# Optimization experiments

Measured on AMD Instinct MI355X. Metric: run time of the kernel, lower is better.

Reference implementation:

```python
import jax, jax.numpy as jnp
import numpy as np

D_MODEL = 1024
N_HEADS = 16
D_K = D_MODEL // N_HEADS  # 64
ROPE_BASE = 10000.0
MASK_FILL = -1e9


def _rope_cos_sin(seq_len, d_k, dtype):
    # inv_freq over even dims, freqs = outer(t, inv_freq): [S, d_k//2]
    inv_freq = 1.0 / (ROPE_BASE ** (jnp.arange(0, d_k, 2, dtype=jnp.float32) / d_k))
    freqs = jnp.arange(seq_len, dtype=jnp.float32)[:, None] * inv_freq[None, :]
    # broadcast to full d_k (rotate_half convention: same freq for x1 and x2 halves)
    cos = jnp.concatenate([jnp.cos(freqs), jnp.cos(freqs)], axis=-1).astype(dtype)
    sin = jnp.concatenate([jnp.sin(freqs), jnp.sin(freqs)], axis=-1).astype(dtype)
    return cos, sin  # each [S, d_k]


def _apply_rope(x, cos, sin):
    # x: [B, H, S, d_k]; rotate_half: (x1, x2) -> (-x2, x1)
    x1, x2 = jnp.split(x, 2, axis=-1)
    rot = jnp.concatenate([-x2, x1], axis=-1)
    return x * cos[None, None] + rot * sin[None, None]


def setup_inputs() -> dict:
    key = jax.random.key(0)
    kx, kqkv, ko = jax.random.split(key, 3)
    x = jax.random.normal(kx, (1, 4096, D_MODEL), dtype=jnp.float32)
    # nn.Linear weight shape [out, in]; y = x @ W.T
    s = 1.0 / np.sqrt(D_MODEL)
    W_qkv = jax.random.uniform(kqkv, (3 * D_MODEL, D_MODEL), jnp.float32, -s, s)
    W_o = jax.random.uniform(ko, (D_MODEL, D_MODEL), jnp.float32, -s, s)
    return {"x": x, "W_qkv": W_qkv, "W_o": W_o}


def reference(x, W_qkv, W_o):
    B, S, _ = x.shape
    qkv = jnp.einsum("bsd,ed->bse", x, W_qkv)  # [B, S, 3*d_model]
    Q, K, V = jnp.split(qkv, 3, axis=-1)
    # [B, S, H, d_k] -> [B, H, S, d_k]
    reshape = lambda t: t.reshape(B, S, N_HEADS, D_K).transpose(0, 2, 1, 3)
    Q, K, V = reshape(Q), reshape(K), reshape(V)
    cos, sin = _rope_cos_sin(S, D_K, x.dtype)
    Q = _apply_rope(Q, cos, sin)
    K = _apply_rope(K, cos, sin)
    scores = jnp.einsum("bhqd,bhkd->bhqk", Q, K) / jnp.sqrt(jnp.asarray(D_K, x.dtype))
    causal = jnp.tril(jnp.ones((S, S), dtype=bool))
    scores = jnp.where(causal[None, None], scores, jnp.asarray(MASK_FILL, x.dtype))
    attn = jax.nn.softmax(scores, axis=-1)  # dropout inactive at inference
    out = jnp.einsum("bhqk,bhkd->bhqd", attn, V)
    out = out.transpose(0, 2, 1, 3).reshape(B, S, D_MODEL)
    return jnp.einsum("bsd,ed->bse", out, W_o)
```

## Files before the change

kernel.cpp:

```cpp
#include <hip/hip_runtime.h>


typedef __attribute__((ext_vector_type(8)))  short  short8;
typedef __attribute__((ext_vector_type(4)))  float  f32x4;
typedef __attribute__((ext_vector_type(16))) float  f32x16;
typedef __attribute__((ext_vector_type(4)))  float  float4v;
typedef __attribute__((ext_vector_type(4)))  unsigned short ushort4v;
typedef __attribute__((ext_vector_type(4)))  unsigned int   uint4v;

#define S_LEN 4096
#define DMODEL 1024
#define NHEADS 16
#define DKH 64

#define QSCALE 0.18033688011112042f

__device__ __forceinline__ unsigned short f2bf(float f) {
  unsigned u = __builtin_bit_cast(unsigned, f);
  u += 0x7FFFu + ((u >> 16) & 1u);
  return (unsigned short)(u >> 16);
}
__device__ __forceinline__ float bf2f(unsigned short h) {
  return __builtin_bit_cast(float, ((unsigned)h) << 16);
}

#define GLDS16(gsrc, ldst)                                                   \
  __builtin_amdgcn_global_load_lds(                                          \
      (const __attribute__((address_space(1))) void*)(gsrc),                 \
      (__attribute__((address_space(3))) void*)(ldst), 16, 0, 0)

__global__ void cvt_bf16_all(const float* __restrict__ x,    unsigned short* __restrict__ xb,
                             const float* __restrict__ wq,   unsigned short* __restrict__ wqb,
                             const float* __restrict__ wo,   unsigned short* __restrict__ wob) {
  int i = blockIdx.x * blockDim.x + threadIdx.x;
  const float* src; unsigned short* dst; int off;
  if (i < 1048576)               { src = x;  dst = xb;  off = i; }
  else if (i < 1048576 + 786432) { src = wq; dst = wqb; off = i - 1048576; }
  else                           { src = wo; dst = wob; off = i - 1048576 - 786432; }
  float4v v = reinterpret_cast<const float4v*>(src)[off];
  ushort4v o;
  o[0] = f2bf(v[0]); o[1] = f2bf(v[1]); o[2] = f2bf(v[2]); o[3] = f2bf(v[3]);
  reinterpret_cast<ushort4v*>(dst)[off] = o;
}

__global__ void rope_table(float2* __restrict__ tab) {
  int id = blockIdx.x * blockDim.x + threadIdx.x;
  int s = id >> 5, i = id & 31;
  float inv = expf(-(float)(2 * i) * (9.2103403719761836f / 64.0f));
  float ang = (float)s * inv;
  float sn, cs;
  sincosf(ang, &sn, &cs);
  tab[id] = make_float2(cs, sn);
}

__global__ __launch_bounds__(256) void gemm_qkv(const unsigned short* __restrict__ A,
                                                const unsigned short* __restrict__ B,
                                                const float2* __restrict__ tab,
                                                unsigned short* __restrict__ Qr,
                                                unsigned short* __restrict__ Kr,
                                                unsigned short* __restrict__ vtmp) {
  const int K = 1024;
  __shared__ __align__(16) unsigned short As[128 * 32];
  __shared__ __align__(16) unsigned short Bs[128 * 32];

  const int tid = threadIdx.x;
  const int l = tid & 63, w = tid >> 6;
  const int wr = w >> 1, wc = w & 1;
  const int bm = blockIdx.y * 128, bn = blockIdx.x * 128;
  const int lr = l & 15, lk = (l >> 4) * 8;

  f32x4 acc[4][4] = {};

  const unsigned short* Ag0 = A + (size_t)(bm + (tid >> 2)) * K + (tid & 3) * 8;
  const unsigned short* Ag1 = A + (size_t)(bm + 64 + (tid >> 2)) * K + (tid & 3) * 8;
  const unsigned short* Bg0 = B + (size_t)(bn + (tid >> 2)) * K + (tid & 3) * 8;
  const unsigned short* Bg1 = B + (size_t)(bn + 64 + (tid >> 2)) * K + (tid & 3) * 8;
  unsigned short* Ad0 = As + tid * 8;
  unsigned short* Ad1 = As + (tid + 256) * 8;
  unsigned short* Bd0 = Bs + tid * 8;
  unsigned short* Bd1 = Bs + (tid + 256) * 8;

  const unsigned short* Afr = As + (wr * 64 + lr) * 32 + lk;
  const unsigned short* Bfr = Bs + (wc * 64 + lr) * 32 + lk;

  for (int k0 = 0; k0 < K; k0 += 32) {
    GLDS16(Ag0 + k0, Ad0);
    GLDS16(Ag1 + k0, Ad1);
    GLDS16(Bg0 + k0, Bd0);
    GLDS16(Bg1 + k0, Bd1);
    __syncthreads();

    short8 af[4], bfr[4];
#pragma unroll
    for (int mi = 0; mi < 4; mi++) af[mi]  = *(const short8*)(Afr + mi * 16 * 32);
#pragma unroll
    for (int ni = 0; ni < 4; ni++) bfr[ni] = *(const short8*)(Bfr + ni * 16 * 32);

#pragma unroll
    for (int mi = 0; mi < 4; mi++)
#pragma unroll
      for (int ni = 0; ni < 4; ni++)
        acc[mi][ni] = __builtin_amdgcn_mfma_f32_16x16x32_bf16(af[mi], bfr[ni],
                                                              acc[mi][ni], 0, 0, 0);
    __syncthreads();
  }

  const int row0 = bm + wr * 64 + (l >> 4) * 4;
  const int region = bn >> 10;
  if (region < 2) {
    const int base64 = (bn & 1023) + wc * 64;
    const int h = base64 >> 6;
    unsigned short* dst = region ? Kr : Qr;
    const float scale = region ? 1.0f : QSCALE;
    const size_t hb = (size_t)h * S_LEN * DKH;
#pragma unroll
    for (int mi = 0; mi < 4; mi++)
#pragma unroll
      for (int jj = 0; jj < 4; jj++) {
        const int s = row0 + mi * 16 + jj;
        const float2 cs0 = tab[s * 32 + lr];
        const float2 cs1 = tab[s * 32 + lr + 16];
        const float x1 = acc[mi][0][jj], x2 = acc[mi][2][jj];
        const float y1 = acc[mi][1][jj], y2 = acc[mi][3][jj];
        const float o0 = (x1 * cs0.x - x2 * cs0.y) * scale;
        const float o2 = (x2 * cs0.x + x1 * cs0.y) * scale;
        const float o1 = (y1 * cs1.x - y2 * cs1.y) * scale;
        const float o3 = (y2 * cs1.x + y1 * cs1.y) * scale;
        const size_t a = hb + (size_t)s * DKH + lr;
        dst[a]      = f2bf(o0);
        dst[a + 16] = f2bf(o1);
        dst[a + 32] = f2bf(o2);
        dst[a + 48] = f2bf(o3);
      }
  } else {
    const int col0 = (bn - 2048) + wc * 64 + lr;
#pragma unroll
    for (int mi = 0; mi < 4; mi++)
#pragma unroll
      for (int ni = 0; ni < 4; ni++)
#pragma unroll
        for (int jj = 0; jj < 4; jj++)
          vtmp[(size_t)(row0 + mi * 16 + jj) * 1024 + col0 + ni * 16] =
              f2bf(acc[mi][ni][jj]);
  }
}

__global__ __launch_bounds__(256) void gemm_lds_f32(const unsigned short* __restrict__ A,
                                                    const unsigned short* __restrict__ B,
                                                    float* __restrict__ Cp,
                                                    int M, int N, int K) {
  __shared__ __align__(16) unsigned short As[128 * 32];
  __shared__ __align__(16) unsigned short Bs[128 * 32];

  const int tid = threadIdx.x;
  const int l = tid & 63, w = tid >> 6;
  const int wr = w >> 1, wc = w & 1;
  const int bm = blockIdx.y * 128, bn = blockIdx.x * 128;
  const int lr = l & 15, lk = (l >> 4) * 8;

  f32x4 acc[4][4] = {};

  const unsigned short* Ag0 = A + (size_t)(bm + (tid >> 2)) * K + (tid & 3) * 8;
  const unsigned short* Ag1 = A + (size_t)(bm + 64 + (tid >> 2)) * K + (tid & 3) * 8;
  const unsigned short* Bg0 = B + (size_t)(bn + (tid >> 2)) * K + (tid & 3) * 8;
  const unsigned short* Bg1 = B + (size_t)(bn + 64 + (tid >> 2)) * K + (tid & 3) * 8;
  unsigned short* Ad0 = As + tid * 8;
  unsigned short* Ad1 = As + (tid + 256) * 8;
  unsigned short* Bd0 = Bs + tid * 8;
  unsigned short* Bd1 = Bs + (tid + 256) * 8;

  const unsigned short* Afr = As + (wr * 64 + lr) * 32 + lk;
  const unsigned short* Bfr = Bs + (wc * 64 + lr) * 32 + lk;

  for (int k0 = 0; k0 < K; k0 += 32) {
    GLDS16(Ag0 + k0, Ad0);
    GLDS16(Ag1 + k0, Ad1);
    GLDS16(Bg0 + k0, Bd0);
    GLDS16(Bg1 + k0, Bd1);
    __syncthreads();

    short8 af[4], bfr[4];
#pragma unroll
    for (int mi = 0; mi < 4; mi++) af[mi]  = *(const short8*)(Afr + mi * 16 * 32);
#pragma unroll
    for (int ni = 0; ni < 4; ni++) bfr[ni] = *(const short8*)(Bfr + ni * 16 * 32);

#pragma unroll
    for (int mi = 0; mi < 4; mi++)
#pragma unroll
      for (int ni = 0; ni < 4; ni++)
        acc[mi][ni] = __builtin_amdgcn_mfma_f32_16x16x32_bf16(af[mi], bfr[ni],
                                                              acc[mi][ni], 0, 0, 0);
    __syncthreads();
  }

  const int row0 = bm + wr * 64 + (l >> 4) * 4;
  const int col0 = bn + wc * 64 + lr;
#pragma unroll
  for (int mi = 0; mi < 4; mi++)
#pragma unroll
    for (int ni = 0; ni < 4; ni++)
#pragma unroll
      for (int j = 0; j < 4; j++)
        Cp[(size_t)(row0 + mi * 16 + j) * N + (col0 + ni * 16)] = acc[mi][ni][j];
}

__global__ __launch_bounds__(256) void v_transpose(const unsigned short* __restrict__ vtmp,
                                                   unsigned short* __restrict__ Vt) {
  __shared__ unsigned lds[64 * 65];
  const int t  = threadIdx.x;
  const int b  = blockIdx.x;
  const int h  = b >> 6;
  const int s0 = (b & 63) * 64;

  const int sl = t >> 2;
  const int cq = (t & 3) * 16;
  {
    const unsigned short* src = vtmp + (size_t)(s0 + sl) * 1024 + h * 64 + cq;
    short8 v0 = *(const short8*)(src);
    short8 v1 = *(const short8*)(src + 8);
#pragma unroll
    for (int jj = 0; jj < 8; jj++) {
      lds[sl * 65 + cq + jj]     = (unsigned short)v0[jj];
      lds[sl * 65 + cq + 8 + jj] = (unsigned short)v1[jj];
    }
  }
  __syncthreads();

  const int dl = t >> 2;
  const int sq = (t & 3) * 16;
  short8 o0, o1;
#pragma unroll
  for (int k = 0; k < 8; k++) {
    o0[k] = (short)(unsigned short)lds[(sq + k) * 65 + dl];
    o1[k] = (short)(unsigned short)lds[(sq + 8 + k) * 65 + dl];
  }
  unsigned short* dst = Vt + (size_t)(h * 64 + dl) * S_LEN + s0 + sq;
  *(short8*)(dst)     = o0;
  *(short8*)(dst + 8) = o1;
}

__global__ __launch_bounds__(256) void flash_attn_kernel(const unsigned short* __restrict__ Qr,
                                                         const unsigned short* __restrict__ Kr,
                                                         const unsigned short* __restrict__ Vt,
                                                         unsigned short* __restrict__ O) {
  __shared__ __align__(16) char smem[32768];

  const int tid = threadIdx.x;
  const int l  = tid & 63;
  const int w  = tid >> 6;
  const int r  = l & 31;
  const int hi = l >> 5;

  const int bx    = blockIdx.x;
  const int xcd   = bx & 7;
  const int j     = bx >> 3;
  const int h     = xcd * 2 + (j & 1);
  const int qtile = 127 - (j >> 1);
  const int q0    = qtile * 32;

  const unsigned short* Qh = Qr + (size_t)h * S_LEN * DKH;
  const unsigned short* Kh = Kr + (size_t)h * S_LEN * DKH;
  const unsigned short* Vh = Vt + (size_t)h * DKH * S_LEN;

  const int krow  = tid >> 3;
  const int kcE   = (((tid & 7) * 16) ^ ((krow & 7) << 4)) >> 1;
  const size_t kbase = (size_t)krow * DKH + kcE;
  const int vrow  = tid >> 4;
  const int vcE   = (((tid & 15) * 16) ^ ((vrow & 7) << 4)) >> 1;
  const size_t vbase = (size_t)vrow * S_LEN + vcE;

  const int sw      = (r & 7) << 4;
  const int kfbyte  = (w * 32 + r) * 128;
  const int vfbyte0 = r * 256;
  const int vfbyte1 = (r + 32) * 256;
  const int vcol    = w * 64 + hi * 16;

  short8 qf[4];
  {
    const unsigned short* qb = Qh + (size_t)(q0 + r) * 64 + hi * 8;
#pragma unroll
    for (int dc = 0; dc < 4; dc++) qf[dc] = *(const short8*)(qb + dc * 16);
  }

  f32x16 acc0 = {}, acc1 = {};
  float m = -1e30f, lsum = 0.0f;

  const int nwin = (qtile >> 2) + 1;
  for (int it = 0; it < nwin; it++) {
    {
      const unsigned short* Kg = Kh + (size_t)it * 128 * DKH;
      const unsigned short* Vg = Vh + it * 128;
#pragma unroll
      for (int i = 0; i < 4; i++) {
        GLDS16(Kg + kbase + (size_t)i * 32 * DKH, smem + i * 4096 + tid * 16);
        GLDS16(Vg + vbase + (size_t)i * 16 * S_LEN,
               smem + 16384 + i * 4096 + tid * 16);
      }
    }
    __syncthreads();

    const int c = 4 * it + w;
    if (c <= qtile) {
      short8 kf[4], vf[4];
#pragma unroll
      for (int dc = 0; dc < 4; dc++)
        kf[dc] = *(const short8*)(smem + kfbyte + ((dc * 32 + hi * 16) ^ sw));
#pragma unroll
      for (int kc = 0; kc < 2; kc++) {
        vf[kc]     = *(const short8*)(smem + 16384 + vfbyte0 + ((vcol + kc * 32) ^ sw));
        vf[2 + kc] = *(const short8*)(smem + 16384 + vfbyte1 + ((vcol + kc * 32) ^ sw));
      }

      f32x16 st = {};
      __builtin_amdgcn_s_setprio(1);
      st = __builtin_amdgcn_mfma_f32_32x32x16_bf16(kf[0], qf[0], st, 0, 0, 0);
      st = __builtin_amdgcn_mfma_f32_32x32x16_bf16(kf[1], qf[1], st, 0, 0, 0);
      st = __builtin_amdgcn_mfma_f32_32x32x16_bf16(kf[2], qf[2], st, 0, 0, 0);
      st = __builtin_amdgcn_mfma_f32_32x32x16_bf16(kf[3], qf[3], st, 0, 0, 0);
      __builtin_amdgcn_s_setprio(0);

      if (c == qtile) {
#pragma unroll
        for (int reg = 0; reg < 16; reg++) {
          const int koff = (reg & 3) + 8 * (reg >> 2) + 4 * hi;
          if (koff > r) st[reg] = -1e30f;
        }
      }

      float t0 = fmaxf(fmaxf(st[0],  st[1]),  st[2]);
      float t1 = fmaxf(fmaxf(st[3],  st[4]),  st[5]);
      float t2 = fmaxf(fmaxf(st[6],  st[7]),  st[8]);
      float t3 = fmaxf(fmaxf(st[9],  st[10]), st[11]);
      float t4 = fmaxf(fmaxf(st[12], st[13]), st[14]);
      float pm = fmaxf(fmaxf(fmaxf(t0, t1), fmaxf(t2, t3)), fmaxf(t4, st[15]));
      pm = fmaxf(pm, __shfl_xor(pm, 32));

      if (!__all(pm <= m + 8.0f)) {
        float mn  = fmaxf(m, pm);
        float scl = exp2f(m - mn);
        m = mn;
        lsum *= scl;
#pragma unroll
        for (int reg = 0; reg < 16; reg++) { acc0[reg] *= scl; acc1[reg] *= scl; }
      }

      float p[16];
#pragma unroll
      for (int reg = 0; reg < 16; reg++) p[reg] = exp2f(st[reg] - m);

      float s2[8];
#pragma unroll
      for (int i = 0; i < 8; i++) s2[i] = p[2 * i] + p[2 * i + 1];
#pragma unroll
      for (int i = 0; i < 4; i++) s2[i] = s2[i] + s2[i + 4];
      float rs = (s2[0] + s2[2]) + (s2[1] + s2[3]);
      rs += __shfl_xor(rs, 32);
      lsum += rs;

      unsigned wd[8];
#pragma unroll
      for (int i = 0; i < 8; i++) {
        asm("v_cvt_pk_bf16_f32 %0, %1, %2" : "=v"(wd[i]) : "v"(p[2 * i]), "v"(p[2 * i + 1]));
      }
      unsigned pw[8];
#pragma unroll
      for (int i = 0; i < 8; i++) pw[i] = __shfl_xor(wd[i], 32);

      uint4v u0, u1;
      u0[0] = hi ? pw[2] : wd[0];
      u0[1] = hi ? pw[3] : wd[1];
      u0[2] = hi ? wd[2] : pw[0];
      u0[3] = hi ? wd[3] : pw[1];
      u1[0] = hi ? pw[6] : wd[4];
      u1[1] = hi ? pw[7] : wd[5];
      u1[2] = hi ? wd[6] : pw[4];
      u1[3] = hi ? wd[7] : pw[5];
      short8 pa0 = __builtin_bit_cast(short8, u0);
      short8 pa1 = __builtin_bit_cast(short8, u1);

      __builtin_amdgcn_s_setprio(1);
      acc0 = __builtin_amdgcn_mfma_f32_32x32x16_bf16(vf[0], pa0, acc0, 0, 0, 0);
      acc0 = __builtin_amdgcn_mfma_f32_32x32x16_bf16(vf[1], pa1, acc0, 0, 0, 0);
      acc1 = __builtin_amdgcn_mfma_f32_32x32x16_bf16(vf[2], pa0, acc1, 0, 0, 0);
      acc1 = __builtin_amdgcn_mfma_f32_32x32x16_bf16(vf[3], pa1, acc1, 0, 0, 0);
      __builtin_amdgcn_s_setprio(0);
    }
    __syncthreads();
  }

  unsigned (*oaccp)[32][33] = (unsigned (*)[32][33])smem;
  float* mlm = (float*)(smem + 16896);
  float* mll = (float*)(smem + 17408);

  if (hi == 0) { mlm[w * 32 + r] = m; mll[w * 32 + r] = lsum; }
#pragma unroll
  for (int i = 0; i < 8; i++) {
    const int widx = 4 * (i >> 1) + 2 * hi + (i & 1);
    unsigned ua, ub;
    asm("v_cvt_pk_bf16_f32 %0, %1, %2" : "=v"(ua) : "v"(acc0[2 * i]), "v"(acc0[2 * i + 1]));
    asm("v_cvt_pk_bf16_f32 %0, %1, %2" : "=v"(ub) : "v"(acc1[2 * i]), "v"(acc1[2 * i + 1]));
    oaccp[w][r][widx]      = ua;
    oaccp[w][r][16 + widx] = ub;
  }
  __syncthreads();

  const int q  = tid >> 3;
  const int c0 = (tid & 7) * 4;
  const float m0 = mlm[q], m1 = mlm[32 + q], m2 = mlm[64 + q], m3 = mlm[96 + q];
  const float mmax = fmaxf(fmaxf(m0, m1), fmaxf(m2, m3));
  const float sc[4] = {exp2f(m0 - mmax), exp2f(m1 - mmax),
                       exp2f(m2 - mmax), exp2f(m3 - mmax)};
  const float ltot = sc[0] * mll[q] + sc[1] * mll[32 + q] +
                     sc[2] * mll[64 + q] + sc[3] * mll[96 + q];
  const float rinv = 1.0f / ltot;

  float vs[8] = {};
#pragma unroll
  for (int wv = 0; wv < 4; wv++) {
#pragma unroll
    for (int i = 0; i < 4; i++) {
      unsigned u = oaccp[wv][q][c0 + i];
      vs[2 * i]     += sc[wv] * __builtin_bit_cast(float, u << 16);
      vs[2 * i + 1] += sc[wv] * __builtin_bit_cast(float, u & 0xFFFF0000u);
    }
  }
  short8 ov;
#pragma unroll
  for (int i = 0; i < 8; i++) ov[i] = (short)f2bf(vs[i] * rinv);
  *(short8*)(O + (size_t)(q0 + q) * DMODEL + h * 64 + c0 * 2) = ov;
}

extern "C" void kernel_launch(void* const* d_in, const int* in_sizes, int n_in,
                              void* d_out, int out_size, void* d_ws, size_t ws_size,
                              hipStream_t stream) {
  (void)in_sizes; (void)n_in; (void)out_size; (void)ws_size;
  const float* x    = (const float*)d_in[0];
  const float* Wqkv = (const float*)d_in[1];
  const float* Wo   = (const float*)d_in[2];
  float* out = (float*)d_out;

  char* ws = (char*)d_ws;
  const size_t MB = 1u << 20;
  unsigned short* x_bf    = (unsigned short*)(ws + 0 * MB);
  unsigned short* wqkv_bf = (unsigned short*)(ws + 8 * MB);
  unsigned short* wo_bf   = (unsigned short*)(ws + 14 * MB);
  unsigned short* vtmp    = (unsigned short*)(ws + 16 * MB);
  float2*         tab     = (float2*)(ws + 24 * MB);
  unsigned short* Qr      = (unsigned short*)(ws + 40 * MB);
  unsigned short* Kr      = (unsigned short*)(ws + 48 * MB);
  unsigned short* Vt      = (unsigned short*)(ws + 56 * MB);
  unsigned short* Obf     = (unsigned short*)(ws + 64 * MB);

  cvt_bf16_all<<<8192, 256, 0, stream>>>(x, x_bf, Wqkv, wqkv_bf, Wo, wo_bf);
  rope_table<<<512, 256, 0, stream>>>(tab);

  gemm_qkv<<<dim3(3072 / 128, 4096 / 128), 256, 0, stream>>>(x_bf, wqkv_bf, tab,
                                                             Qr, Kr, vtmp);
  v_transpose<<<1024, 256, 0, stream>>>(vtmp, Vt);

  flash_attn_kernel<<<2048, 256, 0, stream>>>(Qr, Kr, Vt, Obf);

  gemm_lds_f32<<<dim3(1024 / 128, 4096 / 128), 256, 0, stream>>>(Obf, wo_bf, out,
                                                                 4096, 1024, 1024);
}
```

Before: 185.4 us.

## Double-buffer K/V tiles and split flash-attention block into two query tiles

Each block now covers 64 queries using two wave pairs, and each wave pair splits the keys of a 64-key window. The 64-key K/V windows are double-buffered in LDS, with the next window's global-to-LDS loads issued before the current window is computed, so load latency overlaps with MFMA work. The final combine merges two partial softmax states per query row instead of four. This halves the grid, which reduces parallelism across CUs, and spreads the per-window K/V reuse over two query tiles.

After: 177.6 us. -4.2%, faster.

```diff
diff --git a/kernel.cpp b/kernel.cpp
--- a/kernel.cpp
+++ b/kernel.cpp
@@ -244,41 +244,44 @@
                                                          const unsigned short* __restrict__ Kr,
                                                          const unsigned short* __restrict__ Vt,
                                                          unsigned short* __restrict__ O) {
-  __shared__ __align__(16) char smem[32768];
+  __shared__ __align__(16) char smem[2][16384];
 
   const int tid = threadIdx.x;
   const int l  = tid & 63;
   const int w  = tid >> 6;
   const int r  = l & 31;
   const int hi = l >> 5;
+  const int wsub = w >> 1;
+  const int wpar = w & 1;
 
   const int bx    = blockIdx.x;
   const int xcd   = bx & 7;
   const int j     = bx >> 3;
   const int h     = xcd * 2 + (j & 1);
-  const int qtile = 127 - (j >> 1);
-  const int q0    = qtile * 32;
+  const int jj    = 63 - (j >> 1);
+  const int q0    = jj * 64;
 
   const unsigned short* Qh = Qr + (size_t)h * S_LEN * DKH;
   const unsigned short* Kh = Kr + (size_t)h * S_LEN * DKH;
   const unsigned short* Vh = Vt + (size_t)h * DKH * S_LEN;
 
-  const int krow  = tid >> 3;
-  const int kcE   = (((tid & 7) * 16) ^ ((krow & 7) << 4)) >> 1;
-  const size_t kbase = (size_t)krow * DKH + kcE;
-  const int vrow  = tid >> 4;
-  const int vcE   = (((tid & 15) * 16) ^ ((vrow & 7) << 4)) >> 1;
-  const size_t vbase = (size_t)vrow * S_LEN + vcE;
+  const int qtile_w = 2 * jj + wsub;
+  const int qbase   = q0 + wsub * 32;
+
+  const int srow = tid >> 3;
+  const int scol = (((tid & 7) * 16) ^ ((srow & 7) << 4)) >> 1;
+  const size_t kbase = (size_t)srow * DKH + scol;
+  const size_t vbase = (size_t)srow * S_LEN + scol;
 
   const int sw      = (r & 7) << 4;
-  const int kfbyte  = (w * 32 + r) * 128;
-  const int vfbyte0 = r * 256;
-  const int vfbyte1 = (r + 32) * 256;
-  const int vcol    = w * 64 + hi * 16;
+  const int kfbyte  = (wpar * 32 + r) * 128;
+  const int vfbyte0 = r * 128;
+  const int vfbyte1 = (r + 32) * 128;
+  const int vcol    = wpar * 64 + hi * 16;
 
   short8 qf[4];
   {
-    const unsigned short* qb = Qh + (size_t)(q0 + r) * 64 + hi * 8;
+    const unsigned short* qb = Qh + (size_t)(qbase + r) * 64 + hi * 8;
 #pragma unroll
     for (int dc = 0; dc < 4; dc++) qf[dc] = *(const short8*)(qb + dc * 16);
   }
@@ -286,30 +289,39 @@
   f32x16 acc0 = {}, acc1 = {};
   float m = -1e30f, lsum = 0.0f;
 
-  const int nwin = (qtile >> 2) + 1;
+  const int nwin = jj + 1;
+
+#pragma unroll
+  for (int i = 0; i < 2; i++) {
+    GLDS16(Kh + kbase + (size_t)i * 32 * DKH,   smem[0] + i * 4096 + tid * 16);
+    GLDS16(Vh + vbase + (size_t)i * 32 * S_LEN, smem[0] + 8192 + i * 4096 + tid * 16);
+  }
+  __syncthreads();
+
+  int buf = 0;
   for (int it = 0; it < nwin; it++) {
-    {
-      const unsigned short* Kg = Kh + (size_t)it * 128 * DKH;
-      const unsigned short* Vg = Vh + it * 128;
-#pragma unroll
-      for (int i = 0; i < 4; i++) {
-        GLDS16(Kg + kbase + (size_t)i * 32 * DKH, smem + i * 4096 + tid * 16);
-        GLDS16(Vg + vbase + (size_t)i * 16 * S_LEN,
-               smem + 16384 + i * 4096 + tid * 16);
+    if (it + 1 < nwin) {
+      char* sd = smem[buf ^ 1];
+      const unsigned short* Kg = Kh + (size_t)(it + 1) * 64 * DKH;
+      const unsigned short* Vg = Vh + (size_t)(it + 1) * 64;
+#pragma unroll
+      for (int i = 0; i < 2; i++) {
+        GLDS16(Kg + kbase + (size_t)i * 32 * DKH,   sd + i * 4096 + tid * 16);
+        GLDS16(Vg + vbase + (size_t)i * 32 * S_LEN, sd + 8192 + i * 4096 + tid * 16);
       }
     }
-    __syncthreads();
-
-    const int c = 4 * it + w;
-    if (c <= qtile) {
+
+    const char* sm = smem[buf];
+    const int c = 2 * it + wpar;
+    if (c <= qtile_w) {
       short8 kf[4], vf[4];
 #pragma unroll
       for (int dc = 0; dc < 4; dc++)
-        kf[dc] = *(const short8*)(smem + kfbyte + ((dc * 32 + hi * 16) ^ sw));
+        kf[dc] = *(const short8*)(sm + kfbyte + ((dc * 32 + hi * 16) ^ sw));
 #pragma unroll
       for (int kc = 0; kc < 2; kc++) {
-        vf[kc]     = *(const short8*)(smem + 16384 + vfbyte0 + ((vcol + kc * 32) ^ sw));
-        vf[2 + kc] = *(const short8*)(smem + 16384 + vfbyte1 + ((vcol + kc * 32) ^ sw));
+        vf[kc]     = *(const short8*)(sm + 8192 + vfbyte0 + ((vcol + kc * 32) ^ sw));
+        vf[2 + kc] = *(const short8*)(sm + 8192 + vfbyte1 + ((vcol + kc * 32) ^ sw));
       }
 
       f32x16 st = {};
@@ -320,7 +332,7 @@
       st = __builtin_amdgcn_mfma_f32_32x32x16_bf16(kf[3], qf[3], st, 0, 0, 0);
       __builtin_amdgcn_s_setprio(0);
 
-      if (c == qtile) {
+      if (c == qtile_w) {
 #pragma unroll
         for (int reg = 0; reg < 16; reg++) {
           const int koff = (reg & 3) + 8 * (reg >> 2) + 4 * hi;
@@ -386,12 +398,14 @@
       acc1 = __builtin_amdgcn_mfma_f32_32x32x16_bf16(vf[3], pa1, acc1, 0, 0, 0);
       __builtin_amdgcn_s_setprio(0);
     }
+
     __syncthreads();
+    buf ^= 1;
   }
 
   unsigned (*oaccp)[32][33] = (unsigned (*)[32][33])smem;
-  float* mlm = (float*)(smem + 16896);
-  float* mll = (float*)(smem + 17408);
+  float* mlm = (float*)((char*)smem + 16896);
+  float* mll = (float*)((char*)smem + 17408);
 
   if (hi == 0) { mlm[w * 32 + r] = m; mll[w * 32 + r] = lsum; }
 #pragma unroll
@@ -405,30 +419,37 @@
   }
   __syncthreads();
 
-  const int q  = tid >> 3;
-  const int c0 = (tid & 7) * 4;
-  const float m0 = mlm[q], m1 = mlm[32 + q], m2 = mlm[64 + q], m3 = mlm[96 + q];
-  const float mmax = fmaxf(fmaxf(m0, m1), fmaxf(m2, m3));
-  const float sc[4] = {exp2f(m0 - mmax), exp2f(m1 - mmax),
-                       exp2f(m2 - mmax), exp2f(m3 - mmax)};
-  const float ltot = sc[0] * mll[q] + sc[1] * mll[32 + q] +
-                     sc[2] * mll[64 + q] + sc[3] * mll[96 + q];
+  const int st  = tid >> 7;
+  const int rem = tid & 127;
+  const int q   = rem >> 2;
+  const int c0  = (rem & 3) * 8;
+  const int w0  = 2 * st, w1 = 2 * st + 1;
+
+  const float m0 = mlm[w0 * 32 + q], m1 = mlm[w1 * 32 + q];
+  const float mmax = fmaxf(m0, m1);
+  const float sc0 = exp2f(m0 - mmax), sc1 = exp2f(m1 - mmax);
+  const float ltot = sc0 * mll[w0 * 32 + q] + sc1 * mll[w1 * 32 + q];
   const float rinv = 1.0f / ltot;
 
-  float vs[8] = {};
-#pragma unroll
-  for (int wv = 0; wv < 4; wv++) {
-#pragma unroll
-    for (int i = 0; i < 4; i++) {
-      unsigned u = oaccp[wv][q][c0 + i];
-      vs[2 * i]     += sc[wv] * __builtin_bit_cast(float, u << 16);
-      vs[2 * i + 1] += sc[wv] * __builtin_bit_cast(float, u & 0xFFFF0000u);
-    }
-  }
-  short8 ov;
-#pragma unroll
-  for (int i = 0; i < 8; i++) ov[i] = (short)f2bf(vs[i] * rinv);
-  *(short8*)(O + (size_t)(q0 + q) * DMODEL + h * 64 + c0 * 2) = ov;
+  float vs[16];
+#pragma unroll
+  for (int i = 0; i < 8; i++) {
+    unsigned ua = oaccp[w0][q][c0 + i];
+    unsigned ub = oaccp[w1][q][c0 + i];
+    vs[2 * i]     = sc0 * __builtin_bit_cast(float, ua << 16)
+                  + sc1 * __builtin_bit_cast(float, ub << 16);
+    vs[2 * i + 1] = sc0 * __builtin_bit_cast(float, ua & 0xFFFF0000u)
+                  + sc1 * __builtin_bit_cast(float, ub & 0xFFFF0000u);
+  }
+  short8 ov0, ov1;
+#pragma unroll
+  for (int i = 0; i < 8; i++) {
+    ov0[i] = (short)f2bf(vs[i] * rinv);
+    ov1[i] = (short)f2bf(vs[8 + i] * rinv);
+  }
+  unsigned short* op = O + (size_t)(q0 + st * 32 + q) * DMODEL + h * 64 + c0 * 2;
+  *(short8*)(op)     = ov0;
+  *(short8*)(op + 8) = ov1;
 }
 
 extern "C" void kernel_launch(void* const* d_in, const int* in_sizes, int n_in,
@@ -459,7 +480,7 @@
                                                              Qr, Kr, vtmp);
   v_transpose<<<1024, 256, 0, stream>>>(vtmp, Vt);
 
-  flash_attn_kernel<<<2048, 256, 0, stream>>>(Qr, Kr, Vt, Obf);
+  flash_attn_kernel<<<1024, 256, 0, stream>>>(Qr, Kr, Vt, Obf);
 
   gemm_lds_f32<<<dim3(1024 / 128, 4096 / 128), 256, 0, stream>>>(Obf, wo_bf, out,
                                                                  4096, 1024, 1024);
```

## Fuse rope table into cvt, write V transposed in GEMM, pair causal tiles

Applied to the files above, without the earlier changes.

The RoPE table generation moves into the bf16 conversion kernel, and the QKV GEMM now writes V directly in transposed [head, d, seq] layout with 4-element packed stores. This removes the separate rope_table and v_transpose launches along with the vtmp round trip. The flash attention kernel launches half as many blocks, and each block handles two query tiles (tp and 127-tp) so causal work per block is balanced. The costs are strided 8-byte stores for V and longer-running attention blocks with less parallelism per launch.

Result: slower. 201.3 us (+8.6%).

```diff
diff --git a/kernel.cpp b/kernel.cpp
--- a/kernel.cpp
+++ b/kernel.cpp
@@ -29,28 +29,32 @@
       (const __attribute__((address_space(1))) void*)(gsrc),                 \
       (__attribute__((address_space(3))) void*)(ldst), 16, 0, 0)
 
+#define CVT_TOTAL (1048576 + 786432 + 262144)
 __global__ void cvt_bf16_all(const float* __restrict__ x,    unsigned short* __restrict__ xb,
                              const float* __restrict__ wq,   unsigned short* __restrict__ wqb,
-                             const float* __restrict__ wo,   unsigned short* __restrict__ wob) {
+                             const float* __restrict__ wo,   unsigned short* __restrict__ wob,
+                             float2* __restrict__ tab) {
   int i = blockIdx.x * blockDim.x + threadIdx.x;
-  const float* src; unsigned short* dst; int off;
-  if (i < 1048576)               { src = x;  dst = xb;  off = i; }
-  else if (i < 1048576 + 786432) { src = wq; dst = wqb; off = i - 1048576; }
-  else                           { src = wo; dst = wob; off = i - 1048576 - 786432; }
-  float4v v = reinterpret_cast<const float4v*>(src)[off];
-  ushort4v o;
-  o[0] = f2bf(v[0]); o[1] = f2bf(v[1]); o[2] = f2bf(v[2]); o[3] = f2bf(v[3]);
-  reinterpret_cast<ushort4v*>(dst)[off] = o;
-}
-
-__global__ void rope_table(float2* __restrict__ tab) {
-  int id = blockIdx.x * blockDim.x + threadIdx.x;
-  int s = id >> 5, i = id & 31;
-  float inv = expf(-(float)(2 * i) * (9.2103403719761836f / 64.0f));
-  float ang = (float)s * inv;
-  float sn, cs;
-  sincosf(ang, &sn, &cs);
-  tab[id] = make_float2(cs, sn);
+  if (i < CVT_TOTAL) {
+    const float* src; unsigned short* dst; int off;
+    if (i < 1048576)               { src = x;  dst = xb;  off = i; }
+    else if (i < 1048576 + 786432) { src = wq; dst = wqb; off = i - 1048576; }
+    else                           { src = wo; dst = wob; off = i - 1048576 - 786432; }
+    float4v v = reinterpret_cast<const float4v*>(src)[off];
+    ushort4v o;
+    o[0] = f2bf(v[0]); o[1] = f2bf(v[1]); o[2] = f2bf(v[2]); o[3] = f2bf(v[3]);
+    reinterpret_cast<ushort4v*>(dst)[off] = o;
+  } else {
+    int id = i - CVT_TOTAL;
+    if (id < S_LEN * 32) {
+      int s = id >> 5, fi = id & 31;
+      float inv = expf(-(float)(2 * fi) * (9.2103403719761836f / 64.0f));
+      float ang = (float)s * inv;
+      float sn, cs;
+      sincosf(ang, &sn, &cs);
+      tab[id] = make_float2(cs, sn);
+    }
+  }
 }
 
 __global__ __launch_bounds__(256) void gemm_qkv(const unsigned short* __restrict__ A,
@@ -58,7 +62,7 @@
                                                 const float2* __restrict__ tab,
                                                 unsigned short* __restrict__ Qr,
                                                 unsigned short* __restrict__ Kr,
-                                                unsigned short* __restrict__ vtmp) {
+                                                unsigned short* __restrict__ Vt) {
   const int K = 1024;
   __shared__ __align__(16) unsigned short As[128 * 32];
   __shared__ __align__(16) unsigned short Bs[128 * 32];
@@ -133,15 +137,23 @@
         dst[a + 48] = f2bf(o3);
       }
   } else {
-    const int col0 = (bn - 2048) + wc * 64 + lr;
-#pragma unroll
-    for (int mi = 0; mi < 4; mi++)
-#pragma unroll
-      for (int ni = 0; ni < 4; ni++)
-#pragma unroll
-        for (int jj = 0; jj < 4; jj++)
-          vtmp[(size_t)(row0 + mi * 16 + jj) * 1024 + col0 + ni * 16] =
-              f2bf(acc[mi][ni][jj]);
+    const int colh = (bn - 2048) + wc * 64;
+    const int h = colh >> 6;
+    unsigned short* base = Vt + (size_t)h * DKH * S_LEN;
+#pragma unroll
+    for (int mi = 0; mi < 4; mi++) {
+      const int s = row0 + mi * 16;
+#pragma unroll
+      for (int ni = 0; ni < 4; ni++) {
+        const int d = ni * 16 + lr;
+        ushort4v pk;
+        pk[0] = f2bf(acc[mi][ni][0]);
+        pk[1] = f2bf(acc[mi][ni][1]);
+        pk[2] = f2bf(acc[mi][ni][2]);
+        pk[3] = f2bf(acc[mi][ni][3]);
+        *(ushort4v*)(base + (size_t)d * S_LEN + s) = pk;
+      }
+    }
   }
 }
 
@@ -205,41 +217,6 @@
         Cp[(size_t)(row0 + mi * 16 + j) * N + (col0 + ni * 16)] = acc[mi][ni][j];
 }
 
-__global__ __launch_bounds__(256) void v_transpose(const unsigned short* __restrict__ vtmp,
-                                                   unsigned short* __restrict__ Vt) {
-  __shared__ unsigned lds[64 * 65];
-  const int t  = threadIdx.x;
-  const int b  = blockIdx.x;
-  const int h  = b >> 6;
-  const int s0 = (b & 63) * 64;
-
-  const int sl = t >> 2;
-  const int cq = (t & 3) * 16;
-  {
-    const unsigned short* src = vtmp + (size_t)(s0 + sl) * 1024 + h * 64 + cq;
-    short8 v0 = *(const short8*)(src);
-    short8 v1 = *(const short8*)(src + 8);
-#pragma unroll
-    for (int jj = 0; jj < 8; jj++) {
-      lds[sl * 65 + cq + jj]     = (unsigned short)v0[jj];
-      lds[sl * 65 + cq + 8 + jj] = (unsigned short)v1[jj];
-    }
-  }
-  __syncthreads();
-
-  const int dl = t >> 2;
-  const int sq = (t & 3) * 16;
-  short8 o0, o1;
-#pragma unroll
-  for (int k = 0; k < 8; k++) {
-    o0[k] = (short)(unsigned short)lds[(sq + k) * 65 + dl];
-    o1[k] = (short)(unsigned short)lds[(sq + 8 + k) * 65 + dl];
-  }
-  unsigned short* dst = Vt + (size_t)(h * 64 + dl) * S_LEN + s0 + sq;
-  *(short8*)(dst)     = o0;
-  *(short8*)(dst + 8) = o1;
-}
-
 __global__ __launch_bounds__(256) void flash_attn_kernel(const unsigned short* __restrict__ Qr,
                                                          const unsigned short* __restrict__ Kr,
                                                          const unsigned short* __restrict__ Vt,
@@ -252,12 +229,11 @@
   const int r  = l & 31;
   const int hi = l >> 5;
 
-  const int bx    = blockIdx.x;
-  const int xcd   = bx & 7;
-  const int j     = bx >> 3;
-  const int h     = xcd * 2 + (j & 1);
-  const int qtile = 127 - (j >> 1);
-  const int q0    = qtile * 32;
+  const int bx  = blockIdx.x;
+  const int xcd = bx & 7;
+  const int j   = bx >> 3;
+  const int h   = xcd * 2 + (j & 1);
+  const int tp  = j >> 1;
 
   const unsigned short* Qh = Qr + (size_t)h * S_LEN * DKH;
   const unsigned short* Kh = Kr + (size_t)h * S_LEN * DKH;
@@ -276,159 +252,166 @@
   const int vfbyte1 = (r + 32) * 256;
   const int vcol    = w * 64 + hi * 16;
 
-  short8 qf[4];
-  {
-    const unsigned short* qb = Qh + (size_t)(q0 + r) * 64 + hi * 8;
-#pragma unroll
-    for (int dc = 0; dc < 4; dc++) qf[dc] = *(const short8*)(qb + dc * 16);
-  }
-
-  f32x16 acc0 = {}, acc1 = {};
-  float m = -1e30f, lsum = 0.0f;
-
-  const int nwin = (qtile >> 2) + 1;
-  for (int it = 0; it < nwin; it++) {
+  for (int phase = 0; phase < 2; phase++) {
+    const int sub  = phase ? (127 - tp) : tp;
+    const int q0   = sub * 32;
+    const int nwin = (sub >> 2) + 1;
+
+    short8 qf[4];
     {
-      const unsigned short* Kg = Kh + (size_t)it * 128 * DKH;
-      const unsigned short* Vg = Vh + it * 128;
-#pragma unroll
-      for (int i = 0; i < 4; i++) {
-        GLDS16(Kg + kbase + (size_t)i * 32 * DKH, smem + i * 4096 + tid * 16);
-        GLDS16(Vg + vbase + (size_t)i * 16 * S_LEN,
-               smem + 16384 + i * 4096 + tid * 16);
-      }
-    }
-    __syncthreads();
-
-    const int c = 4 * it + w;
-    if (c <= qtile) {
-      short8 kf[4], vf[4];
-#pragma unroll
-      for (int dc = 0; dc < 4; dc++)
-        kf[dc] = *(const short8*)(smem + kfbyte + ((dc * 32 + hi * 16) ^ sw));
-#pragma unroll
-      for (int kc = 0; kc < 2; kc++) {
-        vf[kc]     = *(const short8*)(smem + 16384 + vfbyte0 + ((vcol + kc * 32) ^ sw));
-        vf[2 + kc] = *(const short8*)(smem + 16384 + vfbyte1 + ((vcol + kc * 32) ^ sw));
-      }
-
-      f32x16 st = {};
-      __builtin_amdgcn_s_setprio(1);
-      st = __builtin_amdgcn_mfma_f32_32x32x16_bf16(kf[0], qf[0], st, 0, 0, 0);
-      st = __builtin_amdgcn_mfma_f32_32x32x16_bf16(kf[1], qf[1], st, 0, 0, 0);
-      st = __builtin_amdgcn_mfma_f32_32x32x16_bf16(kf[2], qf[2], st, 0, 0, 0);
-      st = __builtin_amdgcn_mfma_f32_32x32x16_bf16(kf[3], qf[3], st, 0, 0, 0);
-      __builtin_amdgcn_s_setprio(0);
-
-      if (c == qtile) {
-#pragma unroll
-        for (int reg = 0; reg < 16; reg++) {
-          const int koff = (reg & 3) + 8 * (reg >> 2) + 4 * hi;
-          if (koff > r) st[reg] = -1e30f;
+      const unsigned short* qb = Qh + (size_t)(q0 + r) * 64 + hi * 8;
+#pragma unroll
+      for (int dc = 0; dc < 4; dc++) qf[dc] = *(const short8*)(qb + dc * 16);
+    }
+
+    f32x16 acc0 = {}, acc1 = {};
+    float m = -1e30f, lsum = 0.0f;
+
+    for (int it = 0; it < nwin; it++) {
+      {
+        const unsigned short* Kg = Kh + (size_t)it * 128 * DKH;
+        const unsigned short* Vg = Vh + it * 128;
+#pragma unroll
+        for (int i = 0; i < 4; i++) {
+          GLDS16(Kg + kbase + (size_t)i * 32 * DKH, smem + i * 4096 + tid * 16);
+          GLDS16(Vg + vbase + (size_t)i * 16 * S_LEN,
+                 smem + 16384 + i * 4096 + tid * 16);
         }
       }
-
-      float t0 = fmaxf(fmaxf(st[0],  st[1]),  st[2]);
-      float t1 = fmaxf(fmaxf(st[3],  st[4]),  st[5]);
-      float t2 = fmaxf(fmaxf(st[6],  st[7]),  st[8]);
-      float t3 = fmaxf(fmaxf(st[9],  st[10]), st[11]);
-      float t4 = fmaxf(fmaxf(st[12], st[13]), st[14]);
-      float pm = fmaxf(fmaxf(fmaxf(t0, t1), fmaxf(t2, t3)), fmaxf(t4, st[15]));
-      pm = fmaxf(pm, __shfl_xor(pm, 32));
-
-      if (!__all(pm <= m + 8.0f)) {
-        float mn  = fmaxf(m, pm);
-        float scl = exp2f(m - mn);
-        m = mn;
-        lsum *= scl;
-#pragma unroll
-        for (int reg = 0; reg < 16; reg++) { acc0[reg] *= scl; acc1[reg] *= scl; }
+      __syncthreads();
+
+      const int c = 4 * it + w;
+      if (c <= sub) {
+        short8 kf[4], vf[4];
+#pragma unroll
+        for (int dc = 0; dc < 4; dc++)
+          kf[dc] = *(const short8*)(smem + kfbyte + ((dc * 32 + hi * 16) ^ sw));
+#pragma unroll
+        for (int kc = 0; kc < 2; kc++) {
+          vf[kc]     = *(const short8*)(smem + 16384 + vfbyte0 + ((vcol + kc * 32) ^ sw));
+          vf[2 + kc] = *(const short8*)(smem + 16384 + vfbyte1 + ((vcol + kc * 32) ^ sw));
+        }
+
+        f32x16 st = {};
+        __builtin_amdgcn_s_setprio(1);
+        st = __builtin_amdgcn_mfma_f32_32x32x16_bf16(kf[0], qf[0], st, 0, 0, 0);
+        st = __builtin_amdgcn_mfma_f32_32x32x16_bf16(kf[1], qf[1], st, 0, 0, 0);
+        st = __builtin_amdgcn_mfma_f32_32x32x16_bf16(kf[2], qf[2], st, 0, 0, 0);
+        st = __builtin_amdgcn_mfma_f32_32x32x16_bf16(kf[3], qf[3], st, 0, 0, 0);
+        __builtin_amdgcn_s_setprio(0);
+
+        if (c == sub) {
+#pragma unroll
+          for (int reg = 0; reg < 16; reg++) {
+            const int koff = (reg & 3) + 8 * (reg >> 2) + 4 * hi;
+            if (koff > r) st[reg] = -1e30f;
+          }
+        }
+
+        float t0 = fmaxf(fmaxf(st[0],  st[1]),  st[2]);
+        float t1 = fmaxf(fmaxf(st[3],  st[4]),  st[5]);
+        float t2 = fmaxf(fmaxf(st[6],  st[7]),  st[8]);
+        float t3 = fmaxf(fmaxf(st[9],  st[10]), st[11]);
+        float t4 = fmaxf(fmaxf(st[12], st[13]), st[14]);
+        float pm = fmaxf(fmaxf(fmaxf(t0, t1), fmaxf(t2, t3)), fmaxf(t4, st[15]));
+        pm = fmaxf(pm, __shfl_xor(pm, 32));
+
+        if (!__all(pm <= m + 8.0f)) {
+          float mn  = fmaxf(m, pm);
+          float scl = exp2f(m - mn);
+          m = mn;
+          lsum *= scl;
+#pragma unroll
+          for (int reg = 0; reg < 16; reg++) { acc0[reg] *= scl; acc1[reg] *= scl; }
+        }
+
+        float p2[16];
+#pragma unroll
+        for (int reg = 0; reg < 16; reg++) p2[reg] = exp2f(st[reg] - m);
+
+        float s2[8];
+#pragma unroll
+        for (int i = 0; i < 8; i++) s2[i] = p2[2 * i] + p2[2 * i + 1];
+#pragma unroll
+        for (int i = 0; i < 4; i++) s2[i] = s2[i] + s2[i + 4];
+        float rs = (s2[0] + s2[2]) + (s2[1] + s2[3]);
+        rs += __shfl_xor(rs, 32);
+        lsum += rs;
+
+        unsigned wd[8];
+#pragma unroll
+        for (int i = 0; i < 8; i++) {
+          asm("v_cvt_pk_bf16_f32 %0, %1, %2" : "=v"(wd[i]) : "v"(p2[2 * i]), "v"(p2[2 * i + 1]));
+        }
+        unsigned pw[8];
+#pragma unroll
+        for (int i = 0; i < 8; i++) pw[i] = __shfl_xor(wd[i], 32);
+
+        uint4v u0, u1;
+        u0[0] = hi ? pw[2] : wd[0];
+        u0[1] = hi ? pw[3] : wd[1];
+        u0[2] = hi ? wd[2] : pw[0];
+        u0[3] = hi ? wd[3] : pw[1];
+        u1[0] = hi ? pw[6] : wd[4];
+        u1[1] = hi ? pw[7] : wd[5];
+        u1[2] = hi ? wd[6] : pw[4];
+        u1[3] = hi ? wd[7] : pw[5];
+        short8 pa0 = __builtin_bit_cast(short8, u0);
+        short8 pa1 = __builtin_bit_cast(short8, u1);
+
+        __builtin_amdgcn_s_setprio(1);
+        acc0 = __builtin_amdgcn_mfma_f32_32x32x16_bf16(vf[0], pa0, acc0, 0, 0, 0);
+        acc0 = __builtin_amdgcn_mfma_f32_32x32x16_bf16(vf[1], pa1, acc0, 0, 0, 0);
+        acc1 = __builtin_amdgcn_mfma_f32_32x32x16_bf16(vf[2], pa0, acc1, 0, 0, 0);
+        acc1 = __builtin_amdgcn_mfma_f32_32x32x16_bf16(vf[3], pa1, acc1, 0, 0, 0);
+        __builtin_amdgcn_s_setprio(0);
       }
-
-      float p[16];
-#pragma unroll
-      for (int reg = 0; reg < 16; reg++) p[reg] = exp2f(st[reg] - m);
-
-      float s2[8];
-#pragma unroll
-      for (int i = 0; i < 8; i++) s2[i] = p[2 * i] + p[2 * i + 1];
-#pragma unroll
-      for (int i = 0; i < 4; i++) s2[i] = s2[i] + s2[i + 4];
-      float rs = (s2[0] + s2[2]) + (s2[1] + s2[3]);
-      rs += __shfl_xor(rs, 32);
-      lsum += rs;
-
-      unsigned wd[8];
-#pragma unroll
-      for (int i = 0; i < 8; i++) {
-        asm("v_cvt_pk_bf16_f32 %0, %1, %2" : "=v"(wd[i]) : "v"(p[2 * i]), "v"(p[2 * i + 1]));
+      __syncthreads();
+    }
+
+    unsigned (*oaccp)[32][33] = (unsigned (*)[32][33])smem;
+    float* mlm = (float*)(smem + 16896);
+    float* mll = (float*)(smem + 17408);
+
+    if (hi == 0) { mlm[w * 32 + r] = m; mll[w * 32 + r] = lsum; }
+#pragma unroll
+    for (int i = 0; i < 8; i++) {
+      const int widx = 4 * (i >> 1) + 2 * hi + (i & 1);
+      unsigned ua, ub;
+      asm("v_cvt_pk_bf16_f32 %0, %1, %2" : "=v"(ua) : "v"(acc0[2 * i]), "v"(acc0[2 * i + 1]));
+      asm("v_cvt_pk_bf16_f32 %0, %1, %2" : "=v"(ub) : "v"(acc1[2 * i]), "v"(acc1[2 * i + 1]));
+      oaccp[w][r][widx]      = ua;
+      oaccp[w][r][16 + widx] = ub;
+    }
+    __syncthreads();
+
+    const int q  = tid >> 3;
+    const int c0 = (tid & 7) * 4;
+    const float m0 = mlm[q], m1 = mlm[32 + q], m2 = mlm[64 + q], m3 = mlm[96 + q];
+    const float mmax = fmaxf(fmaxf(m0, m1), fmaxf(m2, m3));
+    const float sc[4] = {exp2f(m0 - mmax), exp2f(m1 - mmax),
+                         exp2f(m2 - mmax), exp2f(m3 - mmax)};
+    const float ltot = sc[0] * mll[q] + sc[1] * mll[32 + q] +
+                       sc[2] * mll[64 + q] + sc[3] * mll[96 + q];
+    const float rinv = 1.0f / ltot;
+
+    float vs[8] = {};
+#pragma unroll
+    for (int wv = 0; wv < 4; wv++) {
+#pragma unroll
+      for (int i = 0; i < 4; i++) {
+        unsigned u = oaccp[wv][q][c0 + i];
+        vs[2 * i]     += sc[wv] * __builtin_bit_cast(float, u << 16);
+        vs[2 * i + 1] += sc[wv] * __builtin_bit_cast(float, u & 0xFFFF0000u);
       }
-      unsigned pw[8];
-#pragma unroll
-      for (int i = 0; i < 8; i++) pw[i] = __shfl_xor(wd[i], 32);
-
-      uint4v u0, u1;
-      u0[0] = hi ? pw[2] : wd[0];
-      u0[1] = hi ? pw[3] : wd[1];
-      u0[2] = hi ? wd[2] : pw[0];
-      u0[3] = hi ? wd[3] : pw[1];
-      u1[0] = hi ? pw[6] : wd[4];
-      u1[1] = hi ? pw[7] : wd[5];
-      u1[2] = hi ? wd[6] : pw[4];
-      u1[3] = hi ? wd[7] : pw[5];
-      short8 pa0 = __builtin_bit_cast(short8, u0);
-      short8 pa1 = __builtin_bit_cast(short8, u1);
-
-      __builtin_amdgcn_s_setprio(1);
-      acc0 = __builtin_amdgcn_mfma_f32_32x32x16_bf16(vf[0], pa0, acc0, 0, 0, 0);
-      acc0 = __builtin_amdgcn_mfma_f32_32x32x16_bf16(vf[1], pa1, acc0, 0, 0, 0);
-      acc1 = __builtin_amdgcn_mfma_f32_32x32x16_bf16(vf[2], pa0, acc1, 0, 0, 0);
-      acc1 = __builtin_amdgcn_mfma_f32_32x32x16_bf16(vf[3], pa1, acc1, 0, 0, 0);
-      __builtin_amdgcn_s_setprio(0);
-    }
+    }
+    short8 ov;
+#pragma unroll
+    for (int i = 0; i < 8; i++) ov[i] = (short)f2bf(vs[i] * rinv);
+    *(short8*)(O + (size_t)(q0 + q) * DMODEL + h * 64 + c0 * 2) = ov;
+
     __syncthreads();
   }
-
-  unsigned (*oaccp)[32][33] = (unsigned (*)[32][33])smem;
-  float* mlm = (float*)(smem + 16896);
-  float* mll = (float*)(smem + 17408);
-
-  if (hi == 0) { mlm[w * 32 + r] = m; mll[w * 32 + r] = lsum; }
-#pragma unroll
-  for (int i = 0; i < 8; i++) {
-    const int widx = 4 * (i >> 1) + 2 * hi + (i & 1);
-    unsigned ua, ub;
-    asm("v_cvt_pk_bf16_f32 %0, %1, %2" : "=v"(ua) : "v"(acc0[2 * i]), "v"(acc0[2 * i + 1]));
-    asm("v_cvt_pk_bf16_f32 %0, %1, %2" : "=v"(ub) : "v"(acc1[2 * i]), "v"(acc1[2 * i + 1]));
-    oaccp[w][r][widx]      = ua;
-    oaccp[w][r][16 + widx] = ub;
-  }
-  __syncthreads();
-
-  const int q  = tid >> 3;
-  const int c0 = (tid & 7) * 4;
-  const float m0 = mlm[q], m1 = mlm[32 + q], m2 = mlm[64 + q], m3 = mlm[96 + q];
-  const float mmax = fmaxf(fmaxf(m0, m1), fmaxf(m2, m3));
-  const float sc[4] = {exp2f(m0 - mmax), exp2f(m1 - mmax),
-                       exp2f(m2 - mmax), exp2f(m3 - mmax)};
-  const float ltot = sc[0] * mll[q] + sc[1] * mll[32 + q] +
-                     sc[2] * mll[64 + q] + sc[3] * mll[96 + q];
-  const float rinv = 1.0f / ltot;
-
-  float vs[8] = {};
-#pragma unroll
-  for (int wv = 0; wv < 4; wv++) {
-#pragma unroll
-    for (int i = 0; i < 4; i++) {
-      unsigned u = oaccp[wv][q][c0 + i];
-      vs[2 * i]     += sc[wv] * __builtin_bit_cast(float, u << 16);
-      vs[2 * i + 1] += sc[wv] * __builtin_bit_cast(float, u & 0xFFFF0000u);
-    }
-  }
-  short8 ov;
-#pragma unroll
-  for (int i = 0; i < 8; i++) ov[i] = (short)f2bf(vs[i] * rinv);
-  *(short8*)(O + (size_t)(q0 + q) * DMODEL + h * 64 + c0 * 2) = ov;
 }
 
 extern "C" void kernel_launch(void* const* d_in, const int* in_sizes, int n_in,
@@ -445,21 +428,19 @@
   unsigned short* x_bf    = (unsigned short*)(ws + 0 * MB);
   unsigned short* wqkv_bf = (unsigned short*)(ws + 8 * MB);
   unsigned short* wo_bf   = (unsigned short*)(ws + 14 * MB);
-  unsigned short* vtmp    = (unsigned short*)(ws + 16 * MB);
   float2*         tab     = (float2*)(ws + 24 * MB);
   unsigned short* Qr      = (unsigned short*)(ws + 40 * MB);
   unsigned short* Kr      = (unsigned short*)(ws + 48 * MB);
   unsigned short* Vt      = (unsigned short*)(ws + 56 * MB);
   unsigned short* Obf     = (unsigned short*)(ws + 64 * MB);
 
-  cvt_bf16_all<<<8192, 256, 0, stream>>>(x, x_bf, Wqkv, wqkv_bf, Wo, wo_bf);
-  rope_table<<<512, 256, 0, stream>>>(tab);
+  cvt_bf16_all<<<(CVT_TOTAL + 131072 + 255) / 256, 256, 0, stream>>>(
+      x, x_bf, Wqkv, wqkv_bf, Wo, wo_bf, tab);
 
   gemm_qkv<<<dim3(3072 / 128, 4096 / 128), 256, 0, stream>>>(x_bf, wqkv_bf, tab,
-                                                             Qr, Kr, vtmp);
-  v_transpose<<<1024, 256, 0, stream>>>(vtmp, Vt);
-
-  flash_attn_kernel<<<2048, 256, 0, stream>>>(Qr, Kr, Vt, Obf);
+                                                             Qr, Kr, Vt);
+
+  flash_attn_kernel<<<1024, 256, 0, stream>>>(Qr, Kr, Vt, Obf);
 
   gemm_lds_f32<<<dim3(1024 / 128, 4096 / 128), 256, 0, stream>>>(Obf, wo_bf, out,
                                                                  4096, 1024, 1024);
```
